# Optimization experiments

Hardware: AMD Instinct MI355X
Metric: run time of the kernel (lower is better)

Reference implementation:

```python
import jax, jax.numpy as jnp
import numpy as np

N_NODES = 50000
N_EDGES = 800000
NFEAT, NHID1, NHID2, NHID3, NCLASS = 128, 128, 128, 64, 32


def _glorot(key, fan_in, fan_out):
    lim = 1.0 / np.sqrt(fan_in)
    return jax.random.uniform(key, (fan_in, fan_out), jnp.float32, -lim, lim)


def setup_inputs() -> dict:
    key = jax.random.key(0)
    ks = jax.random.split(key, 12)
    x = jax.random.normal(ks[0], (N_NODES, NFEAT), jnp.float32)
    edge_src = jax.random.randint(ks[1], (N_EDGES,), 0, N_NODES, jnp.int32)
    edge_dst = jax.random.randint(ks[2], (N_EDGES,), 0, N_NODES, jnp.int32)
    edge_val = jax.random.uniform(ks[3], (N_EDGES,), jnp.float32)
    W1 = _glorot(ks[4], NFEAT, NHID1)
    W2 = _glorot(ks[5], NHID1, NHID2)
    W3 = _glorot(ks[6], NHID2, NHID3)
    W4 = _glorot(ks[7], NHID3, NCLASS)
    b1 = jnp.zeros((NHID1,), jnp.float32)
    b2 = jnp.zeros((NHID2,), jnp.float32)
    b3 = jnp.zeros((NHID3,), jnp.float32)
    b4 = jnp.zeros((NCLASS,), jnp.float32)
    return {"x": x, "edge_src": edge_src, "edge_dst": edge_dst, "edge_val": edge_val,
            "W1": W1, "b1": b1, "W2": W2, "b2": b2, "W3": W3, "b3": b3, "W4": W4, "b4": b4}


def _gc_layer(h, W, b, src, dst, val):
    # support = h @ W ; out = adj @ support + b  (adj in COO form)
    support = h @ W                                   # [N, d_out]
    msgs = support[src] * val[:, None]                # [E, d_out] irregular gather
    agg = jax.ops.segment_sum(msgs, dst, num_segments=N_NODES)  # scatter-add
    return agg + b


def reference(x, edge_src, edge_dst, edge_val, W1, b1, W2, b2, W3, b3, W4, b4):
    h = jax.nn.relu(_gc_layer(x, W1, b1, edge_src, edge_dst, edge_val))
    h = jax.nn.relu(_gc_layer(h, W2, b2, edge_src, edge_dst, edge_val))
    h = jax.nn.relu(_gc_layer(h, W3, b3, edge_src, edge_dst, edge_val))
    h = _gc_layer(h, W4, b4, edge_src, edge_dst, edge_val)
    return h
```

## Files before the change

### kernel.cpp

```cpp
#include <hip/hip_runtime.h>

constexpr int NNODES = 50000;
constexpr int NEDGES = 800000;
constexpr int CAP = 64;

typedef __attribute__((ext_vector_type(8))) short short8;
typedef __attribute__((ext_vector_type(8))) unsigned short ushort8;
typedef __attribute__((ext_vector_type(4))) float f32x4;

__device__ __forceinline__ unsigned short f2b(float f) {
    unsigned int u = __float_as_uint(f);
    u += 0x7FFFu + ((u >> 16) & 1u);
    return (unsigned short)(u >> 16);
}
__device__ __forceinline__ float b2f(unsigned short u) {
    return __uint_as_float(((unsigned int)u) << 16);
}

template <int N, int K>
__device__ __forceinline__ void pack_one(int idx, const float* __restrict__ W,
                                         unsigned short* __restrict__ Wp) {
    constexpr int KS = K / 32;
    int j = idx & 7;
    int lane = (idx >> 3) & 63;
    int t = idx >> 9;
    int nt = t / KS, ks = t % KS;
    int n = nt * 16 + (lane & 15);
    int k = ks * 32 + (lane >> 4) * 8 + j;
    Wp[idx] = f2b(W[(size_t)k * N + n]);
}

__global__ __launch_bounds__(256) void prep_kernel(int* __restrict__ cursor,
                                                   const float* __restrict__ W1,
                                                   const float* __restrict__ W2,
                                                   const float* __restrict__ W3,
                                                   const float* __restrict__ W4,
                                                   unsigned short* __restrict__ Wp1,
                                                   unsigned short* __restrict__ Wp2,
                                                   unsigned short* __restrict__ Wp3,
                                                   unsigned short* __restrict__ Wp4) {
    int idx = blockIdx.x * 256 + threadIdx.x;
    if (idx < NNODES) { cursor[idx] = 0; return; }
    int p = idx - NNODES;
    if (p < 16384) pack_one<128, 128>(p, W1, Wp1);
    else if (p < 32768) pack_one<128, 128>(p - 16384, W2, Wp2);
    else if (p < 40960) pack_one<64, 128>(p - 32768, W3, Wp3);
    else if (p < 43008) pack_one<32, 64>(p - 40960, W4, Wp4);
}

constexpr int NPART = 8;
constexpr int PSIZE = NNODES / NPART;
constexpr int FCH = 1024;
constexpr int QCAP = 320;

__global__ __launch_bounds__(256) void fill_kernel(const int* __restrict__ src,
                                                   const int* __restrict__ dst,
                                                   const float* __restrict__ val,
                                                   int* __restrict__ cursor,
                                                   int2* __restrict__ buckets) {
    __shared__ int q_e[QCAP];
    __shared__ int q_d[QCAP];
    __shared__ int qcount;
    if (threadIdx.x == 0) qcount = 0;
    __syncthreads();

    int part = blockIdx.x % NPART;
    int chunk = blockIdx.x / NPART;
    int lo = part * PSIZE, hi = lo + PSIZE;
    int e0 = chunk * FCH + threadIdx.x * 4;

    int4 d4 = make_int4(-1, -1, -1, -1);
    if (e0 + 3 < NEDGES) {
        d4 = *reinterpret_cast<const int4*>(dst + e0);
    } else if (e0 < NEDGES) {
        d4.x = dst[e0];
        if (e0 + 1 < NEDGES) d4.y = dst[e0 + 1];
        if (e0 + 2 < NEDGES) d4.z = dst[e0 + 2];
    }
    int dd[4] = {d4.x, d4.y, d4.z, d4.w};
#pragma unroll
    for (int i = 0; i < 4; ++i) {
        int d = dd[i];
        if (d >= lo && d < hi) {
            int pos = atomicAdd(&qcount, 1);
            if (pos < QCAP) {
                q_e[pos] = e0 + i;
                q_d[pos] = d;
            } else {
                int e = e0 + i;
                int p = atomicAdd(&cursor[d], 1);
                if (p < CAP)
                    buckets[(size_t)d * CAP + p] = make_int2(src[e], __float_as_int(val[e]));
            }
        }
    }
    __syncthreads();

    int n = qcount < QCAP ? qcount : QCAP;
    for (int i = threadIdx.x; i < n; i += 256) {
        int e = q_e[i];
        int d = q_d[i];
        int s = src[e];
        float v = val[e];
        int p = atomicAdd(&cursor[d], 1);
        if (p < CAP)
            buckets[(size_t)d * CAP + p] = make_int2(s, __float_as_int(v));
    }
}

template <int N, int K, bool AF32>
__global__ __launch_bounds__(256) void mfma_gemm_kernel(const void* __restrict__ Hv,
                                                        const unsigned short* __restrict__ Wp,
                                                        unsigned short* __restrict__ Sb) {
    constexpr int NT = N / 16, KS = K / 32;
    const int lane = threadIdx.x & 63;
    const int wave = threadIdx.x >> 6;
    const int waveRow = blockIdx.x * 64 + wave * 16;
    const int m = lane & 15, quad = lane >> 4;
    int arow = waveRow + m;
    if (arow >= NNODES) arow = NNODES - 1;

    f32x4 acc[NT];
#pragma unroll
    for (int nt = 0; nt < NT; ++nt) acc[nt] = (f32x4){0.f, 0.f, 0.f, 0.f};

#pragma unroll
    for (int ks = 0; ks < KS; ++ks) {
        short8 a;
        if (AF32) {
            const float* hp = (const float*)Hv + (size_t)arow * K + ks * 32 + quad * 8;
            float4 a0 = *reinterpret_cast<const float4*>(hp);
            float4 a1 = *reinterpret_cast<const float4*>(hp + 4);
            a[0] = (short)f2b(a0.x); a[1] = (short)f2b(a0.y);
            a[2] = (short)f2b(a0.z); a[3] = (short)f2b(a0.w);
            a[4] = (short)f2b(a1.x); a[5] = (short)f2b(a1.y);
            a[6] = (short)f2b(a1.z); a[7] = (short)f2b(a1.w);
        } else {
            a = *reinterpret_cast<const short8*>(
                (const unsigned short*)Hv + (size_t)arow * K + ks * 32 + quad * 8);
        }
#pragma unroll
        for (int nt = 0; nt < NT; ++nt) {
            short8 b = *reinterpret_cast<const short8*>(Wp + ((nt * KS + ks) * 64 + lane) * 8);
            acc[nt] = __builtin_amdgcn_mfma_f32_16x16x32_bf16(a, b, acc[nt], 0, 0, 0);
        }
    }

#pragma unroll
    for (int reg = 0; reg < 4; ++reg) {
        int grow = waveRow + quad * 4 + reg;
        if (grow < NNODES) {
#pragma unroll
            for (int nt = 0; nt < NT; ++nt)
                Sb[(size_t)grow * N + nt * 16 + m] = f2b(acc[nt][reg]);
        }
    }
}

template <int N, bool BOUT>
__global__ __launch_bounds__(256) void agg_kernel(const unsigned short* __restrict__ Sb,
                                                  const int2* __restrict__ buckets,
                                                  const int* __restrict__ counts,
                                                  const float* __restrict__ bias,
                                                  void* __restrict__ outp) {
    constexpr int NCH = N / 8;
    constexpr int NPB = 256 / NCH;
    int node = blockIdx.x * NPB + threadIdx.x / NCH;
    int cg = threadIdx.x % NCH;
    if (node >= NNODES) return;
    int cnt = counts[node];
    if (cnt > CAP) cnt = CAP;
    const int2* eb = buckets + (size_t)node * CAP;
    float acc[8];
#pragma unroll
    for (int t = 0; t < 8; ++t) acc[t] = bias[cg * 8 + t];

    int j = 0;
    for (; j + 4 <= cnt; j += 4) {
        int4 ea = *reinterpret_cast<const int4*>(eb + j);
        int4 ec = *reinterpret_cast<const int4*>(eb + j + 2);
        const ushort8 m0 = *reinterpret_cast<const ushort8*>(Sb + (size_t)ea.x * N + cg * 8);
        const ushort8 m1 = *reinterpret_cast<const ushort8*>(Sb + (size_t)ea.z * N + cg * 8);
        const ushort8 m2 = *reinterpret_cast<const ushort8*>(Sb + (size_t)ec.x * N + cg * 8);
        const ushort8 m3 = *reinterpret_cast<const ushort8*>(Sb + (size_t)ec.z * N + cg * 8);
        float v0 = __int_as_float(ea.y), v1 = __int_as_float(ea.w);
        float v2 = __int_as_float(ec.y), v3 = __int_as_float(ec.w);
#pragma unroll
        for (int t = 0; t < 8; ++t) {
            acc[t] = fmaf(b2f(m0[t]), v0, acc[t]);
            acc[t] = fmaf(b2f(m1[t]), v1, acc[t]);
            acc[t] = fmaf(b2f(m2[t]), v2, acc[t]);
            acc[t] = fmaf(b2f(m3[t]), v3, acc[t]);
        }
    }
    for (; j < cnt; ++j) {
        int2 e = eb[j];
        float v = __int_as_float(e.y);
        const ushort8 mr = *reinterpret_cast<const ushort8*>(Sb + (size_t)e.x * N + cg * 8);
#pragma unroll
        for (int t = 0; t < 8; ++t) acc[t] = fmaf(b2f(mr[t]), v, acc[t]);
    }

    if (BOUT) {
        ushort8 o;
#pragma unroll
        for (int t = 0; t < 8; ++t) o[t] = f2b(fmaxf(acc[t], 0.f));
        *reinterpret_cast<ushort8*>((unsigned short*)outp + (size_t)node * N + cg * 8) = o;
    } else {
        float* op = (float*)outp + (size_t)node * N + cg * 8;
        *reinterpret_cast<float4*>(op) = make_float4(acc[0], acc[1], acc[2], acc[3]);
        *reinterpret_cast<float4*>(op + 4) = make_float4(acc[4], acc[5], acc[6], acc[7]);
    }
}

extern "C" void kernel_launch(void* const* d_in, const int* in_sizes, int n_in,
                              void* d_out, int out_size, void* d_ws, size_t ws_size,
                              hipStream_t stream) {
    const float* x   = (const float*)d_in[0];
    const int*   src = (const int*)d_in[1];
    const int*   dst = (const int*)d_in[2];
    const float* val = (const float*)d_in[3];
    const float* W1  = (const float*)d_in[4];
    const float* b1  = (const float*)d_in[5];
    const float* W2  = (const float*)d_in[6];
    const float* b2  = (const float*)d_in[7];
    const float* W3  = (const float*)d_in[8];
    const float* b3  = (const float*)d_in[9];
    const float* W4  = (const float*)d_in[10];
    const float* b4  = (const float*)d_in[11];
    float* out = (float*)d_out;

    unsigned short* P = (unsigned short*)d_ws;
    unsigned short* Q = P + (size_t)NNODES * 128;
    int2* buckets = (int2*)(Q + (size_t)NNODES * 128);
    unsigned short* Wp1 = (unsigned short*)(buckets + (size_t)NNODES * CAP);
    unsigned short* Wp2 = Wp1 + 128 * 128;
    unsigned short* Wp3 = Wp2 + 128 * 128;
    unsigned short* Wp4 = Wp3 + 128 * 64;
    int* cursor = (int*)(Wp4 + 64 * 32);

    const dim3 blk(256);
    const int gemmGrid = (NNODES + 63) / 64;
    const int prepGrid = (NNODES + 43008 + 255) / 256;
    const int fillGrid = ((NEDGES + FCH - 1) / FCH) * NPART;

    prep_kernel<<<prepGrid, blk, 0, stream>>>(cursor, W1, W2, W3, W4, Wp1, Wp2, Wp3, Wp4);
    fill_kernel<<<fillGrid, blk, 0, stream>>>(src, dst, val, cursor, buckets);

    mfma_gemm_kernel<128, 128, true><<<gemmGrid, blk, 0, stream>>>(x, Wp1, Q);
    agg_kernel<128, true><<<(NNODES + 15) / 16, blk, 0, stream>>>(Q, buckets, cursor, b1, P);
    mfma_gemm_kernel<128, 128, false><<<gemmGrid, blk, 0, stream>>>(P, Wp2, Q);
    agg_kernel<128, true><<<(NNODES + 15) / 16, blk, 0, stream>>>(Q, buckets, cursor, b2, P);
    mfma_gemm_kernel<64, 128, false><<<gemmGrid, blk, 0, stream>>>(P, Wp3, Q);
    agg_kernel<64, true><<<(NNODES + 31) / 32, blk, 0, stream>>>(Q, buckets, cursor, b3, P);
    mfma_gemm_kernel<32, 64, false><<<gemmGrid, blk, 0, stream>>>(P, Wp4, Q);
    agg_kernel<32, false><<<(NNODES + 63) / 64, blk, 0, stream>>>(Q, buckets, cursor, b4, out);
}
```

Measured before the change: 254.0 us.

## Fuse aggregation of each layer with next layer's MFMA GEMM via LDS tile

Each aggregation (gather, scale, bias, ReLU) now writes its 64-node bf16 result into shared memory, and the same block immediately runs the next layer's MFMA GEMM from that tile. This removes the global round trip of the intermediate hidden activations and three kernel launches. In exchange, the gather now uses 4 threads per node with wider per-thread channel slices (more registers, fewer threads per node, less memory-level parallelism), and the GEMM waits on a block barrier.

Result: slower. 266.7 us (+5.0%).

```diff
diff --git a/kernel.cpp b/kernel.cpp
--- a/kernel.cpp
+++ b/kernel.cpp
@@ -108,10 +108,10 @@
     }
 }
 
-template <int N, int K, bool AF32>
-__global__ __launch_bounds__(256) void mfma_gemm_kernel(const void* __restrict__ Hv,
-                                                        const unsigned short* __restrict__ Wp,
-                                                        unsigned short* __restrict__ Sb) {
+template <int N, int K>
+__global__ __launch_bounds__(256) void mfma_gemm_f32_kernel(const float* __restrict__ H,
+                                                            const unsigned short* __restrict__ Wp,
+                                                            unsigned short* __restrict__ Sb) {
     constexpr int NT = N / 16, KS = K / 32;
     const int lane = threadIdx.x & 63;
     const int wave = threadIdx.x >> 6;
@@ -126,19 +126,14 @@
 
 #pragma unroll
     for (int ks = 0; ks < KS; ++ks) {
+        const float* hp = H + (size_t)arow * K + ks * 32 + quad * 8;
+        float4 a0 = *reinterpret_cast<const float4*>(hp);
+        float4 a1 = *reinterpret_cast<const float4*>(hp + 4);
         short8 a;
-        if (AF32) {
-            const float* hp = (const float*)Hv + (size_t)arow * K + ks * 32 + quad * 8;
-            float4 a0 = *reinterpret_cast<const float4*>(hp);
-            float4 a1 = *reinterpret_cast<const float4*>(hp + 4);
-            a[0] = (short)f2b(a0.x); a[1] = (short)f2b(a0.y);
-            a[2] = (short)f2b(a0.z); a[3] = (short)f2b(a0.w);
-            a[4] = (short)f2b(a1.x); a[5] = (short)f2b(a1.y);
-            a[6] = (short)f2b(a1.z); a[7] = (short)f2b(a1.w);
-        } else {
-            a = *reinterpret_cast<const short8*>(
-                (const unsigned short*)Hv + (size_t)arow * K + ks * 32 + quad * 8);
-        }
+        a[0] = (short)f2b(a0.x); a[1] = (short)f2b(a0.y);
+        a[2] = (short)f2b(a0.z); a[3] = (short)f2b(a0.w);
+        a[4] = (short)f2b(a1.x); a[5] = (short)f2b(a1.y);
+        a[6] = (short)f2b(a1.z); a[7] = (short)f2b(a1.w);
 #pragma unroll
         for (int nt = 0; nt < NT; ++nt) {
             short8 b = *reinterpret_cast<const short8*>(Wp + ((nt * KS + ks) * 64 + lane) * 8);
@@ -157,16 +152,116 @@
     }
 }
 
-template <int N, bool BOUT>
-__global__ __launch_bounds__(256) void agg_kernel(const unsigned short* __restrict__ Sb,
-                                                  const int2* __restrict__ buckets,
-                                                  const int* __restrict__ counts,
-                                                  const float* __restrict__ bias,
-                                                  void* __restrict__ outp) {
-    constexpr int NCH = N / 8;
-    constexpr int NPB = 256 / NCH;
-    int node = blockIdx.x * NPB + threadIdx.x / NCH;
-    int cg = threadIdx.x % NCH;
+template <int NIN, int NOUT>
+__global__ __launch_bounds__(256) void layer_kernel(const unsigned short* __restrict__ Sprev,
+                                                    const int2* __restrict__ buckets,
+                                                    const int* __restrict__ counts,
+                                                    const float* __restrict__ bias,
+                                                    const unsigned short* __restrict__ Wp,
+                                                    unsigned short* __restrict__ Snext) {
+    constexpr int KS = NIN / 32;
+    constexpr int NT = NOUT / 16;
+    constexpr int CPT = NIN / 4;
+    constexpr int NC8 = CPT / 8;
+    constexpr int LROW = NIN + 8;
+    __shared__ unsigned short htile[64 * LROW];
+
+    const int tid = threadIdx.x;
+    const int nodeBase = blockIdx.x * 64;
+
+    {
+        int nl = tid >> 2;
+        int q = tid & 3;
+        int node = nodeBase + nl;
+        float acc[CPT];
+        if (node < NNODES) {
+#pragma unroll
+            for (int t = 0; t < CPT; ++t) acc[t] = bias[q * CPT + t];
+            int cnt = counts[node];
+            if (cnt > CAP) cnt = CAP;
+            const int2* eb = buckets + (size_t)node * CAP;
+            int j = 0;
+            for (; j + 2 <= cnt; j += 2) {
+                int4 ee = *reinterpret_cast<const int4*>(eb + j);
+                const unsigned short* r0 = Sprev + (size_t)ee.x * NIN + q * CPT;
+                const unsigned short* r1 = Sprev + (size_t)ee.z * NIN + q * CPT;
+                ushort8 m0[NC8], m1[NC8];
+#pragma unroll
+                for (int c = 0; c < NC8; ++c) m0[c] = *reinterpret_cast<const ushort8*>(r0 + c * 8);
+#pragma unroll
+                for (int c = 0; c < NC8; ++c) m1[c] = *reinterpret_cast<const ushort8*>(r1 + c * 8);
+                float v0 = __int_as_float(ee.y), v1 = __int_as_float(ee.w);
+#pragma unroll
+                for (int c = 0; c < NC8; ++c)
+#pragma unroll
+                    for (int t = 0; t < 8; ++t) {
+                        acc[c * 8 + t] = fmaf(b2f(m0[c][t]), v0, acc[c * 8 + t]);
+                        acc[c * 8 + t] = fmaf(b2f(m1[c][t]), v1, acc[c * 8 + t]);
+                    }
+            }
+            if (j < cnt) {
+                int2 e = eb[j];
+                float v = __int_as_float(e.y);
+                const unsigned short* r0 = Sprev + (size_t)e.x * NIN + q * CPT;
+#pragma unroll
+                for (int c = 0; c < NC8; ++c) {
+                    ushort8 mr = *reinterpret_cast<const ushort8*>(r0 + c * 8);
+#pragma unroll
+                    for (int t = 0; t < 8; ++t)
+                        acc[c * 8 + t] = fmaf(b2f(mr[t]), v, acc[c * 8 + t]);
+                }
+            }
+        } else {
+#pragma unroll
+            for (int t = 0; t < CPT; ++t) acc[t] = 0.f;
+        }
+        unsigned short* lrow = &htile[nl * LROW + q * CPT];
+#pragma unroll
+        for (int c = 0; c < NC8; ++c) {
+            ushort8 o;
+#pragma unroll
+            for (int t = 0; t < 8; ++t) o[t] = f2b(fmaxf(acc[c * 8 + t], 0.f));
+            *reinterpret_cast<ushort8*>(lrow + c * 8) = o;
+        }
+    }
+    __syncthreads();
+
+    {
+        const int lane = tid & 63, wave = tid >> 6;
+        const int m = lane & 15, quad = lane >> 4;
+        const int lrow = wave * 16 + m;
+        f32x4 acc[NT];
+#pragma unroll
+        for (int nt = 0; nt < NT; ++nt) acc[nt] = (f32x4){0.f, 0.f, 0.f, 0.f};
+#pragma unroll
+        for (int ks = 0; ks < KS; ++ks) {
+            short8 a = *reinterpret_cast<const short8*>(&htile[lrow * LROW + ks * 32 + quad * 8]);
+#pragma unroll
+            for (int nt = 0; nt < NT; ++nt) {
+                short8 b = *reinterpret_cast<const short8*>(Wp + ((nt * KS + ks) * 64 + lane) * 8);
+                acc[nt] = __builtin_amdgcn_mfma_f32_16x16x32_bf16(a, b, acc[nt], 0, 0, 0);
+            }
+        }
+#pragma unroll
+        for (int reg = 0; reg < 4; ++reg) {
+            int grow = nodeBase + wave * 16 + quad * 4 + reg;
+            if (grow < NNODES) {
+#pragma unroll
+                for (int nt = 0; nt < NT; ++nt)
+                    Snext[(size_t)grow * NOUT + nt * 16 + m] = f2b(acc[nt][reg]);
+            }
+        }
+    }
+}
+
+__global__ __launch_bounds__(256) void agg_out_kernel(const unsigned short* __restrict__ Sb,
+                                                      const int2* __restrict__ buckets,
+                                                      const int* __restrict__ counts,
+                                                      const float* __restrict__ bias,
+                                                      float* __restrict__ outp) {
+    constexpr int N = 32;
+    int node = blockIdx.x * 64 + threadIdx.x / 4;
+    int cg = threadIdx.x % 4;
     if (node >= NNODES) return;
     int cnt = counts[node];
     if (cnt > CAP) cnt = CAP;
@@ -201,16 +296,9 @@
         for (int t = 0; t < 8; ++t) acc[t] = fmaf(b2f(mr[t]), v, acc[t]);
     }
 
-    if (BOUT) {
-        ushort8 o;
-#pragma unroll
-        for (int t = 0; t < 8; ++t) o[t] = f2b(fmaxf(acc[t], 0.f));
-        *reinterpret_cast<ushort8*>((unsigned short*)outp + (size_t)node * N + cg * 8) = o;
-    } else {
-        float* op = (float*)outp + (size_t)node * N + cg * 8;
-        *reinterpret_cast<float4*>(op) = make_float4(acc[0], acc[1], acc[2], acc[3]);
-        *reinterpret_cast<float4*>(op + 4) = make_float4(acc[4], acc[5], acc[6], acc[7]);
-    }
+    float* op = outp + (size_t)node * N + cg * 8;
+    *reinterpret_cast<float4*>(op) = make_float4(acc[0], acc[1], acc[2], acc[3]);
+    *reinterpret_cast<float4*>(op + 4) = make_float4(acc[4], acc[5], acc[6], acc[7]);
 }
 
 extern "C" void kernel_launch(void* const* d_in, const int* in_sizes, int n_in,
@@ -240,19 +328,16 @@
     int* cursor = (int*)(Wp4 + 64 * 32);
 
     const dim3 blk(256);
-    const int gemmGrid = (NNODES + 63) / 64;
+    const int grid64 = (NNODES + 63) / 64;
     const int prepGrid = (NNODES + 43008 + 255) / 256;
     const int fillGrid = ((NEDGES + FCH - 1) / FCH) * NPART;
 
     prep_kernel<<<prepGrid, blk, 0, stream>>>(cursor, W1, W2, W3, W4, Wp1, Wp2, Wp3, Wp4);
     fill_kernel<<<fillGrid, blk, 0, stream>>>(src, dst, val, cursor, buckets);
 
-    mfma_gemm_kernel<128, 128, true><<<gemmGrid, blk, 0, stream>>>(x, Wp1, Q);
-    agg_kernel<128, true><<<(NNODES + 15) / 16, blk, 0, stream>>>(Q, buckets, cursor, b1, P);
-    mfma_gemm_kernel<128, 128, false><<<gemmGrid, blk, 0, stream>>>(P, Wp2, Q);
-    agg_kernel<128, true><<<(NNODES + 15) / 16, blk, 0, stream>>>(Q, buckets, cursor, b2, P);
-    mfma_gemm_kernel<64, 128, false><<<gemmGrid, blk, 0, stream>>>(P, Wp3, Q);
-    agg_kernel<64, true><<<(NNODES + 31) / 32, blk, 0, stream>>>(Q, buckets, cursor, b3, P);
-    mfma_gemm_kernel<32, 64, false><<<gemmGrid, blk, 0, stream>>>(P, Wp4, Q);
-    agg_kernel<32, false><<<(NNODES + 63) / 64, blk, 0, stream>>>(Q, buckets, cursor, b4, out);
-}
+    mfma_gemm_f32_kernel<128, 128><<<grid64, blk, 0, stream>>>(x, Wp1, Q);
+    layer_kernel<128, 128><<<grid64, blk, 0, stream>>>(Q, buckets, cursor, b1, Wp2, P);
+    layer_kernel<128, 64><<<grid64, blk, 0, stream>>>(P, buckets, cursor, b2, Wp3, Q);
+    layer_kernel<64, 32><<<grid64, blk, 0, stream>>>(Q, buckets, cursor, b3, Wp4, P);
+    agg_out_kernel<<<grid64, blk, 0, stream>>>(P, buckets, cursor, b4, out);
+}
```

## Fuse all GCN stages into one persistent cooperative kernel with grid syncs

Applied to the files above, without the earlier changes.

Replaces the ten separate launches with one persistent cooperative kernel. Blocks loop over work items for each stage, with grid-wide barriers between stages. The bucket fill and the first-layer GEMM now share one stage, since they are independent. The aim is to remove per-launch overhead and tail gaps between small kernels. The cost is grid.sync barriers, a fixed grid of at most 1024 blocks, and occupancy capped by launch bounds. The old multi-kernel path is kept as a fallback if the cooperative launch fails.

Measured after the change: 794.7 us. 3.13x slower.

```diff
diff --git a/kernel.cpp b/kernel.cpp
--- a/kernel.cpp
+++ b/kernel.cpp
@@ -1,8 +1,20 @@
 #include <hip/hip_runtime.h>
+#include <hip/hip_cooperative_groups.h>
+
+namespace cg = cooperative_groups;
 
 constexpr int NNODES = 50000;
 constexpr int NEDGES = 800000;
 constexpr int CAP = 64;
+
+constexpr int NPART = 8;
+constexpr int PSIZE = NNODES / NPART;
+constexpr int FCH = 1024;
+constexpr int QCAP = 320;
+
+constexpr int FILL_ITEMS = ((NEDGES + FCH - 1) / FCH) * NPART;
+constexpr int TILE_ITEMS = (NNODES + 63) / 64;
+constexpr int PREP_TOT = NNODES + 43008;
 
 typedef __attribute__((ext_vector_type(8))) short short8;
 typedef __attribute__((ext_vector_type(8))) unsigned short ushort8;
@@ -30,16 +42,11 @@
     Wp[idx] = f2b(W[(size_t)k * N + n]);
 }
 
-__global__ __launch_bounds__(256) void prep_kernel(int* __restrict__ cursor,
-                                                   const float* __restrict__ W1,
-                                                   const float* __restrict__ W2,
-                                                   const float* __restrict__ W3,
-                                                   const float* __restrict__ W4,
-                                                   unsigned short* __restrict__ Wp1,
-                                                   unsigned short* __restrict__ Wp2,
-                                                   unsigned short* __restrict__ Wp3,
-                                                   unsigned short* __restrict__ Wp4) {
-    int idx = blockIdx.x * 256 + threadIdx.x;
+__device__ __forceinline__ void prep_elem(int idx, int* __restrict__ cursor,
+                                          const float* W1, const float* W2,
+                                          const float* W3, const float* W4,
+                                          unsigned short* Wp1, unsigned short* Wp2,
+                                          unsigned short* Wp3, unsigned short* Wp4) {
     if (idx < NNODES) { cursor[idx] = 0; return; }
     int p = idx - NNODES;
     if (p < 16384) pack_one<128, 128>(p, W1, Wp1);
@@ -48,24 +55,17 @@
     else if (p < 43008) pack_one<32, 64>(p - 40960, W4, Wp4);
 }
 
-constexpr int NPART = 8;
-constexpr int PSIZE = NNODES / NPART;
-constexpr int FCH = 1024;
-constexpr int QCAP = 320;
-
-__global__ __launch_bounds__(256) void fill_kernel(const int* __restrict__ src,
-                                                   const int* __restrict__ dst,
-                                                   const float* __restrict__ val,
-                                                   int* __restrict__ cursor,
-                                                   int2* __restrict__ buckets) {
-    __shared__ int q_e[QCAP];
-    __shared__ int q_d[QCAP];
-    __shared__ int qcount;
-    if (threadIdx.x == 0) qcount = 0;
+__device__ __forceinline__ void fill_item(int w, const int* __restrict__ src,
+                                          const int* __restrict__ dst,
+                                          const float* __restrict__ val,
+                                          int* __restrict__ cursor,
+                                          int2* __restrict__ buckets,
+                                          int* q_e, int* q_d, int* qcount) {
+    if (threadIdx.x == 0) *qcount = 0;
     __syncthreads();
 
-    int part = blockIdx.x % NPART;
-    int chunk = blockIdx.x / NPART;
+    int part = w % NPART;
+    int chunk = w / NPART;
     int lo = part * PSIZE, hi = lo + PSIZE;
     int e0 = chunk * FCH + threadIdx.x * 4;
 
@@ -82,7 +82,7 @@
     for (int i = 0; i < 4; ++i) {
         int d = dd[i];
         if (d >= lo && d < hi) {
-            int pos = atomicAdd(&qcount, 1);
+            int pos = atomicAdd(qcount, 1);
             if (pos < QCAP) {
                 q_e[pos] = e0 + i;
                 q_d[pos] = d;
@@ -96,7 +96,7 @@
     }
     __syncthreads();
 
-    int n = qcount < QCAP ? qcount : QCAP;
+    int n = *qcount < QCAP ? *qcount : QCAP;
     for (int i = threadIdx.x; i < n; i += 256) {
         int e = q_e[i];
         int d = q_d[i];
@@ -109,13 +109,13 @@
 }
 
 template <int N, int K, bool AF32>
-__global__ __launch_bounds__(256) void mfma_gemm_kernel(const void* __restrict__ Hv,
-                                                        const unsigned short* __restrict__ Wp,
-                                                        unsigned short* __restrict__ Sb) {
+__device__ __forceinline__ void gemm_item(int t, const void* __restrict__ Hv,
+                                          const unsigned short* __restrict__ Wp,
+                                          unsigned short* __restrict__ Sb) {
     constexpr int NT = N / 16, KS = K / 32;
     const int lane = threadIdx.x & 63;
     const int wave = threadIdx.x >> 6;
-    const int waveRow = blockIdx.x * 64 + wave * 16;
+    const int waveRow = t * 64 + wave * 16;
     const int m = lane & 15, quad = lane >> 4;
     int arow = waveRow + m;
     if (arow >= NNODES) arow = NNODES - 1;
@@ -158,31 +158,31 @@
 }
 
 template <int N, bool BOUT>
-__global__ __launch_bounds__(256) void agg_kernel(const unsigned short* __restrict__ Sb,
-                                                  const int2* __restrict__ buckets,
-                                                  const int* __restrict__ counts,
-                                                  const float* __restrict__ bias,
-                                                  void* __restrict__ outp) {
+__device__ __forceinline__ void agg_item(int w, const unsigned short* __restrict__ Sb,
+                                         const int2* __restrict__ buckets,
+                                         const int* __restrict__ counts,
+                                         const float* __restrict__ bias,
+                                         void* __restrict__ outp) {
     constexpr int NCH = N / 8;
     constexpr int NPB = 256 / NCH;
-    int node = blockIdx.x * NPB + threadIdx.x / NCH;
-    int cg = threadIdx.x % NCH;
+    int node = w * NPB + threadIdx.x / NCH;
+    int cgi = threadIdx.x % NCH;
     if (node >= NNODES) return;
     int cnt = counts[node];
     if (cnt > CAP) cnt = CAP;
     const int2* eb = buckets + (size_t)node * CAP;
     float acc[8];
 #pragma unroll
-    for (int t = 0; t < 8; ++t) acc[t] = bias[cg * 8 + t];
+    for (int t = 0; t < 8; ++t) acc[t] = bias[cgi * 8 + t];
 
     int j = 0;
     for (; j + 4 <= cnt; j += 4) {
         int4 ea = *reinterpret_cast<const int4*>(eb + j);
         int4 ec = *reinterpret_cast<const int4*>(eb + j + 2);
-        const ushort8 m0 = *reinterpret_cast<const ushort8*>(Sb + (size_t)ea.x * N + cg * 8);
-        const ushort8 m1 = *reinterpret_cast<const ushort8*>(Sb + (size_t)ea.z * N + cg * 8);
-        const ushort8 m2 = *reinterpret_cast<const ushort8*>(Sb + (size_t)ec.x * N + cg * 8);
-        const ushort8 m3 = *reinterpret_cast<const ushort8*>(Sb + (size_t)ec.z * N + cg * 8);
+        const ushort8 m0 = *reinterpret_cast<const ushort8*>(Sb + (size_t)ea.x * N + cgi * 8);
+        const ushort8 m1 = *reinterpret_cast<const ushort8*>(Sb + (size_t)ea.z * N + cgi * 8);
+        const ushort8 m2 = *reinterpret_cast<const ushort8*>(Sb + (size_t)ec.x * N + cgi * 8);
+        const ushort8 m3 = *reinterpret_cast<const ushort8*>(Sb + (size_t)ec.z * N + cgi * 8);
         float v0 = __int_as_float(ea.y), v1 = __int_as_float(ea.w);
         float v2 = __int_as_float(ec.y), v3 = __int_as_float(ec.w);
 #pragma unroll
@@ -196,7 +196,7 @@
     for (; j < cnt; ++j) {
         int2 e = eb[j];
         float v = __int_as_float(e.y);
-        const ushort8 mr = *reinterpret_cast<const ushort8*>(Sb + (size_t)e.x * N + cg * 8);
+        const ushort8 mr = *reinterpret_cast<const ushort8*>(Sb + (size_t)e.x * N + cgi * 8);
 #pragma unroll
         for (int t = 0; t < 8; ++t) acc[t] = fmaf(b2f(mr[t]), v, acc[t]);
     }
@@ -205,12 +205,99 @@
         ushort8 o;
 #pragma unroll
         for (int t = 0; t < 8; ++t) o[t] = f2b(fmaxf(acc[t], 0.f));
-        *reinterpret_cast<ushort8*>((unsigned short*)outp + (size_t)node * N + cg * 8) = o;
+        *reinterpret_cast<ushort8*>((unsigned short*)outp + (size_t)node * N + cgi * 8) = o;
     } else {
-        float* op = (float*)outp + (size_t)node * N + cg * 8;
+        float* op = (float*)outp + (size_t)node * N + cgi * 8;
         *reinterpret_cast<float4*>(op) = make_float4(acc[0], acc[1], acc[2], acc[3]);
         *reinterpret_cast<float4*>(op + 4) = make_float4(acc[4], acc[5], acc[6], acc[7]);
     }
+}
+
+__global__ __launch_bounds__(256, 4) void mono_kernel(
+        const float* __restrict__ x, const int* __restrict__ src,
+        const int* __restrict__ dst, const float* __restrict__ val,
+        const float* __restrict__ W1, const float* __restrict__ b1,
+        const float* __restrict__ W2, const float* __restrict__ b2,
+        const float* __restrict__ W3, const float* __restrict__ b3,
+        const float* __restrict__ W4, const float* __restrict__ b4,
+        float* __restrict__ out,
+        unsigned short* __restrict__ P, unsigned short* __restrict__ Q,
+        int2* __restrict__ buckets,
+        unsigned short* __restrict__ Wp1, unsigned short* __restrict__ Wp2,
+        unsigned short* __restrict__ Wp3, unsigned short* __restrict__ Wp4,
+        int* __restrict__ cursor) {
+    cg::grid_group grid = cg::this_grid();
+    const int nb = gridDim.x;
+    __shared__ int q_e[QCAP];
+    __shared__ int q_d[QCAP];
+    __shared__ int qcount;
+
+    for (int base = blockIdx.x * 256; base < PREP_TOT; base += nb * 256) {
+        int idx = base + threadIdx.x;
+        if (idx < PREP_TOT)
+            prep_elem(idx, cursor, W1, W2, W3, W4, Wp1, Wp2, Wp3, Wp4);
+    }
+    grid.sync();
+
+    for (int w = blockIdx.x; w < FILL_ITEMS + TILE_ITEMS; w += nb) {
+        if (w < FILL_ITEMS) fill_item(w, src, dst, val, cursor, buckets, q_e, q_d, &qcount);
+        else gemm_item<128, 128, true>(w - FILL_ITEMS, x, Wp1, Q);
+    }
+    grid.sync();
+
+    for (int w = blockIdx.x; w < (NNODES + 15) / 16; w += nb)
+        agg_item<128, true>(w, Q, buckets, cursor, b1, P);
+    grid.sync();
+
+    for (int w = blockIdx.x; w < TILE_ITEMS; w += nb)
+        gemm_item<128, 128, false>(w, P, Wp2, Q);
+    grid.sync();
+
+    for (int w = blockIdx.x; w < (NNODES + 15) / 16; w += nb)
+        agg_item<128, true>(w, Q, buckets, cursor, b2, P);
+    grid.sync();
+
+    for (int w = blockIdx.x; w < TILE_ITEMS; w += nb)
+        gemm_item<64, 128, false>(w, P, Wp3, Q);
+    grid.sync();
+
+    for (int w = blockIdx.x; w < (NNODES + 31) / 32; w += nb)
+        agg_item<64, true>(w, Q, buckets, cursor, b3, P);
+    grid.sync();
+
+    for (int w = blockIdx.x; w < TILE_ITEMS; w += nb)
+        gemm_item<32, 64, false>(w, P, Wp4, Q);
+    grid.sync();
+
+    for (int w = blockIdx.x; w < (NNODES + 63) / 64; w += nb)
+        agg_item<32, false>(w, Q, buckets, cursor, b4, out);
+}
+
+__global__ __launch_bounds__(256) void prep_kernel(int* cursor,
+        const float* W1, const float* W2, const float* W3, const float* W4,
+        unsigned short* Wp1, unsigned short* Wp2, unsigned short* Wp3, unsigned short* Wp4) {
+    int idx = blockIdx.x * 256 + threadIdx.x;
+    if (idx < PREP_TOT) prep_elem(idx, cursor, W1, W2, W3, W4, Wp1, Wp2, Wp3, Wp4);
+}
+
+__global__ __launch_bounds__(256) void fill_kernel(const int* src, const int* dst,
+        const float* val, int* cursor, int2* buckets) {
+    __shared__ int q_e[QCAP];
+    __shared__ int q_d[QCAP];
+    __shared__ int qcount;
+    fill_item(blockIdx.x, src, dst, val, cursor, buckets, q_e, q_d, &qcount);
+}
+
+template <int N, int K, bool AF32>
+__global__ __launch_bounds__(256) void gemm_kernel(const void* Hv,
+        const unsigned short* Wp, unsigned short* Sb) {
+    gemm_item<N, K, AF32>(blockIdx.x, Hv, Wp, Sb);
+}
+
+template <int N, bool BOUT>
+__global__ __launch_bounds__(256) void agg_kernel(const unsigned short* Sb,
+        const int2* buckets, const int* counts, const float* bias, void* outp) {
+    agg_item<N, BOUT>(blockIdx.x, Sb, buckets, counts, bias, outp);
 }
 
 extern "C" void kernel_launch(void* const* d_in, const int* in_sizes, int n_in,
@@ -239,20 +326,33 @@
     unsigned short* Wp4 = Wp3 + 128 * 64;
     int* cursor = (int*)(Wp4 + 64 * 32);
 
+    int blocksPerCU = 0;
+    hipError_t occErr = hipOccupancyMaxActiveBlocksPerMultiprocessor(
+        &blocksPerCU, (const void*)mono_kernel, 256, 0);
+    if (occErr == hipSuccess && blocksPerCU > 0) {
+        int grid = blocksPerCU * 256;
+        if (grid > 1024) grid = 1024;
+        void* args[] = {(void*)&x, (void*)&src, (void*)&dst, (void*)&val,
+                        (void*)&W1, (void*)&b1, (void*)&W2, (void*)&b2,
+                        (void*)&W3, (void*)&b3, (void*)&W4, (void*)&b4,
+                        (void*)&out, (void*)&P, (void*)&Q, (void*)&buckets,
+                        (void*)&Wp1, (void*)&Wp2, (void*)&Wp3, (void*)&Wp4,
+                        (void*)&cursor};
+        hipError_t err = hipLaunchCooperativeKernel((const void*)mono_kernel,
+                                                    dim3(grid), dim3(256), args, 0, stream);
+        if (err == hipSuccess) return;
+    }
+
     const dim3 blk(256);
-    const int gemmGrid = (NNODES + 63) / 64;
-    const int prepGrid = (NNODES + 43008 + 255) / 256;
-    const int fillGrid = ((NEDGES + FCH - 1) / FCH) * NPART;
-
-    prep_kernel<<<prepGrid, blk, 0, stream>>>(cursor, W1, W2, W3, W4, Wp1, Wp2, Wp3, Wp4);
-    fill_kernel<<<fillGrid, blk, 0, stream>>>(src, dst, val, cursor, buckets);
-
-    mfma_gemm_kernel<128, 128, true><<<gemmGrid, blk, 0, stream>>>(x, Wp1, Q);
+    prep_kernel<<<(PREP_TOT + 255) / 256, blk, 0, stream>>>(cursor, W1, W2, W3, W4,
+                                                            Wp1, Wp2, Wp3, Wp4);
+    fill_kernel<<<FILL_ITEMS, blk, 0, stream>>>(src, dst, val, cursor, buckets);
+    gemm_kernel<128, 128, true><<<TILE_ITEMS, blk, 0, stream>>>(x, Wp1, Q);
     agg_kernel<128, true><<<(NNODES + 15) / 16, blk, 0, stream>>>(Q, buckets, cursor, b1, P);
-    mfma_gemm_kernel<128, 128, false><<<gemmGrid, blk, 0, stream>>>(P, Wp2, Q);
+    gemm_kernel<128, 128, false><<<TILE_ITEMS, blk, 0, stream>>>(P, Wp2, Q);
     agg_kernel<128, true><<<(NNODES + 15) / 16, blk, 0, stream>>>(Q, buckets, cursor, b2, P);
-    mfma_gemm_kernel<64, 128, false><<<gemmGrid, blk, 0, stream>>>(P, Wp3, Q);
+    gemm_kernel<64, 128, false><<<TILE_ITEMS, blk, 0, stream>>>(P, Wp3, Q);
     agg_kernel<64, true><<<(NNODES + 31) / 32, blk, 0, stream>>>(Q, buckets, cursor, b3, P);
-    mfma_gemm_kernel<32, 64, false><<<gemmGrid, blk, 0, stream>>>(P, Wp4, Q);
+    gemm_kernel<32, 64, false><<<TILE_ITEMS, blk, 0, stream>>>(P, Wp4, Q);
     agg_kernel<32, false><<<(NNODES + 63) / 64, blk, 0, stream>>>(Q, buckets, cursor, b4, out);
 }
```

## Fuse aggregation with next-layer GEMM and merge edge fill with first GEMM

Applied to the files above, without the earlier changes.

Each aggregation kernel now writes its ReLU'd bf16 result into a shared-memory tile and immediately runs the next layer's MFMA GEMM on it. This removes the round trip of hidden activations through global memory and cuts the launch count. The edge-bucket fill and the first-layer GEMM are merged into one launch, with extra blocks doing the GEMM tiles so both run concurrently. The cost is small 16- or 32-row GEMM tiles per block, with the weights re-read from global by every block and more LDS use per block.

Measured after the change: 227.2 us. 1.12x faster.

```diff
diff --git a/kernel.cpp b/kernel.cpp
--- a/kernel.cpp
+++ b/kernel.cpp
@@ -3,6 +3,15 @@
 constexpr int NNODES = 50000;
 constexpr int NEDGES = 800000;
 constexpr int CAP = 64;
+
+constexpr int NPART = 8;
+constexpr int PSIZE = NNODES / NPART;
+constexpr int FCH = 1024;
+constexpr int QCAP = 320;
+
+constexpr int FILL_ITEMS = ((NEDGES + FCH - 1) / FCH) * NPART;
+constexpr int TILE_ITEMS = (NNODES + 63) / 64;
+constexpr int PREP_TOT = NNODES + 43008;
 
 typedef __attribute__((ext_vector_type(8))) short short8;
 typedef __attribute__((ext_vector_type(8))) unsigned short ushort8;
@@ -31,91 +40,27 @@
 }
 
 __global__ __launch_bounds__(256) void prep_kernel(int* __restrict__ cursor,
-                                                   const float* __restrict__ W1,
-                                                   const float* __restrict__ W2,
-                                                   const float* __restrict__ W3,
-                                                   const float* __restrict__ W4,
-                                                   unsigned short* __restrict__ Wp1,
-                                                   unsigned short* __restrict__ Wp2,
-                                                   unsigned short* __restrict__ Wp3,
-                                                   unsigned short* __restrict__ Wp4) {
+        const float* __restrict__ W1, const float* __restrict__ W2,
+        const float* __restrict__ W3, const float* __restrict__ W4,
+        unsigned short* __restrict__ Wp1, unsigned short* __restrict__ Wp2,
+        unsigned short* __restrict__ Wp3, unsigned short* __restrict__ Wp4) {
     int idx = blockIdx.x * 256 + threadIdx.x;
     if (idx < NNODES) { cursor[idx] = 0; return; }
     int p = idx - NNODES;
     if (p < 16384) pack_one<128, 128>(p, W1, Wp1);
     else if (p < 32768) pack_one<128, 128>(p - 16384, W2, Wp2);
     else if (p < 40960) pack_one<64, 128>(p - 32768, W3, Wp3);
-    else if (p < 43008) pack_one<32, 64>(p - 40960, W4, Wp4);
-}
-
-constexpr int NPART = 8;
-constexpr int PSIZE = NNODES / NPART;
-constexpr int FCH = 1024;
-constexpr int QCAP = 320;
-
-__global__ __launch_bounds__(256) void fill_kernel(const int* __restrict__ src,
-                                                   const int* __restrict__ dst,
-                                                   const float* __restrict__ val,
-                                                   int* __restrict__ cursor,
-                                                   int2* __restrict__ buckets) {
-    __shared__ int q_e[QCAP];
-    __shared__ int q_d[QCAP];
-    __shared__ int qcount;
-    if (threadIdx.x == 0) qcount = 0;
-    __syncthreads();
-
-    int part = blockIdx.x % NPART;
-    int chunk = blockIdx.x / NPART;
-    int lo = part * PSIZE, hi = lo + PSIZE;
-    int e0 = chunk * FCH + threadIdx.x * 4;
-
-    int4 d4 = make_int4(-1, -1, -1, -1);
-    if (e0 + 3 < NEDGES) {
-        d4 = *reinterpret_cast<const int4*>(dst + e0);
-    } else if (e0 < NEDGES) {
-        d4.x = dst[e0];
-        if (e0 + 1 < NEDGES) d4.y = dst[e0 + 1];
-        if (e0 + 2 < NEDGES) d4.z = dst[e0 + 2];
-    }
-    int dd[4] = {d4.x, d4.y, d4.z, d4.w};
-#pragma unroll
-    for (int i = 0; i < 4; ++i) {
-        int d = dd[i];
-        if (d >= lo && d < hi) {
-            int pos = atomicAdd(&qcount, 1);
-            if (pos < QCAP) {
-                q_e[pos] = e0 + i;
-                q_d[pos] = d;
-            } else {
-                int e = e0 + i;
-                int p = atomicAdd(&cursor[d], 1);
-                if (p < CAP)
-                    buckets[(size_t)d * CAP + p] = make_int2(src[e], __float_as_int(val[e]));
-            }
-        }
-    }
-    __syncthreads();
-
-    int n = qcount < QCAP ? qcount : QCAP;
-    for (int i = threadIdx.x; i < n; i += 256) {
-        int e = q_e[i];
-        int d = q_d[i];
-        int s = src[e];
-        float v = val[e];
-        int p = atomicAdd(&cursor[d], 1);
-        if (p < CAP)
-            buckets[(size_t)d * CAP + p] = make_int2(s, __float_as_int(v));
-    }
+    else if (p < 43008 && p >= 40960) pack_one<32, 64>(p - 40960, W4, Wp4);
 }
 
 template <int N, int K, bool AF32>
-__global__ __launch_bounds__(256) void mfma_gemm_kernel(const void* __restrict__ Hv,
-                                                        const unsigned short* __restrict__ Wp,
-                                                        unsigned short* __restrict__ Sb) {
+__device__ __forceinline__ void gemm_item(int t, const void* __restrict__ Hv,
+                                          const unsigned short* __restrict__ Wp,
+                                          unsigned short* __restrict__ Sb) {
     constexpr int NT = N / 16, KS = K / 32;
     const int lane = threadIdx.x & 63;
     const int wave = threadIdx.x >> 6;
-    const int waveRow = blockIdx.x * 64 + wave * 16;
+    const int waveRow = t * 64 + wave * 16;
     const int m = lane & 15, quad = lane >> 4;
     int arow = waveRow + m;
     if (arow >= NNODES) arow = NNODES - 1;
@@ -157,16 +102,160 @@
     }
 }
 
-template <int N, bool BOUT>
-__global__ __launch_bounds__(256) void agg_kernel(const unsigned short* __restrict__ Sb,
-                                                  const int2* __restrict__ buckets,
-                                                  const int* __restrict__ counts,
-                                                  const float* __restrict__ bias,
-                                                  void* __restrict__ outp) {
-    constexpr int NCH = N / 8;
-    constexpr int NPB = 256 / NCH;
-    int node = blockIdx.x * NPB + threadIdx.x / NCH;
-    int cg = threadIdx.x % NCH;
+__global__ __launch_bounds__(256) void fill_gemm1_kernel(
+        const int* __restrict__ src, const int* __restrict__ dst,
+        const float* __restrict__ val, int* __restrict__ cursor,
+        int2* __restrict__ buckets,
+        const float* __restrict__ x, const unsigned short* __restrict__ Wp1,
+        unsigned short* __restrict__ Q) {
+    __shared__ int q_e[QCAP];
+    __shared__ int q_d[QCAP];
+    __shared__ int qcount;
+
+    if (blockIdx.x >= FILL_ITEMS) {
+        gemm_item<128, 128, true>(blockIdx.x - FILL_ITEMS, x, Wp1, Q);
+        return;
+    }
+
+    if (threadIdx.x == 0) qcount = 0;
+    __syncthreads();
+
+    int part = blockIdx.x % NPART;
+    int chunk = blockIdx.x / NPART;
+    int lo = part * PSIZE, hi = lo + PSIZE;
+    int e0 = chunk * FCH + threadIdx.x * 4;
+
+    int4 d4 = make_int4(-1, -1, -1, -1);
+    if (e0 + 3 < NEDGES) {
+        d4 = *reinterpret_cast<const int4*>(dst + e0);
+    } else if (e0 < NEDGES) {
+        d4.x = dst[e0];
+        if (e0 + 1 < NEDGES) d4.y = dst[e0 + 1];
+        if (e0 + 2 < NEDGES) d4.z = dst[e0 + 2];
+    }
+    int dd[4] = {d4.x, d4.y, d4.z, d4.w};
+#pragma unroll
+    for (int i = 0; i < 4; ++i) {
+        int d = dd[i];
+        if (d >= lo && d < hi) {
+            int pos = atomicAdd(&qcount, 1);
+            if (pos < QCAP) {
+                q_e[pos] = e0 + i;
+                q_d[pos] = d;
+            } else {
+                int e = e0 + i;
+                int p = atomicAdd(&cursor[d], 1);
+                if (p < CAP)
+                    buckets[(size_t)d * CAP + p] = make_int2(src[e], __float_as_int(val[e]));
+            }
+        }
+    }
+    __syncthreads();
+
+    int n = qcount < QCAP ? qcount : QCAP;
+    for (int i = threadIdx.x; i < n; i += 256) {
+        int e = q_e[i];
+        int d = q_d[i];
+        int s = src[e];
+        float v = val[e];
+        int p = atomicAdd(&cursor[d], 1);
+        if (p < CAP)
+            buckets[(size_t)d * CAP + p] = make_int2(s, __float_as_int(v));
+    }
+}
+
+template <int NIN, int NOUT>
+__global__ __launch_bounds__(256) void agg_gemm_kernel(
+        const unsigned short* __restrict__ Sprev, const int2* __restrict__ buckets,
+        const int* __restrict__ counts, const float* __restrict__ bias,
+        const unsigned short* __restrict__ Wp, unsigned short* __restrict__ Snext) {
+    constexpr int NCH = NIN / 8;
+    constexpr int R = 256 / NCH;
+    constexpr int LROW = NIN + 8;
+    constexpr int KS = NIN / 32;
+    constexpr int NT = NOUT / 16;
+    constexpr int RT = R / 16;
+    constexpr int TILES = RT * NT;
+    __shared__ unsigned short htile[R * LROW];
+
+    const int nodeBase = blockIdx.x * R;
+
+    {
+        int nl = threadIdx.x / NCH;
+        int cg = threadIdx.x % NCH;
+        int node = nodeBase + nl;
+        float acc[8];
+        if (node < NNODES) {
+#pragma unroll
+            for (int t = 0; t < 8; ++t) acc[t] = bias[cg * 8 + t];
+            int cnt = counts[node];
+            if (cnt > CAP) cnt = CAP;
+            const int2* eb = buckets + (size_t)node * CAP;
+            int j = 0;
+            for (; j + 4 <= cnt; j += 4) {
+                int4 ea = *reinterpret_cast<const int4*>(eb + j);
+                int4 ec = *reinterpret_cast<const int4*>(eb + j + 2);
+                const ushort8 m0 = *reinterpret_cast<const ushort8*>(Sprev + (size_t)ea.x * NIN + cg * 8);
+                const ushort8 m1 = *reinterpret_cast<const ushort8*>(Sprev + (size_t)ea.z * NIN + cg * 8);
+                const ushort8 m2 = *reinterpret_cast<const ushort8*>(Sprev + (size_t)ec.x * NIN + cg * 8);
+                const ushort8 m3 = *reinterpret_cast<const ushort8*>(Sprev + (size_t)ec.z * NIN + cg * 8);
+                float v0 = __int_as_float(ea.y), v1 = __int_as_float(ea.w);
+                float v2 = __int_as_float(ec.y), v3 = __int_as_float(ec.w);
+#pragma unroll
+                for (int t = 0; t < 8; ++t) {
+                    acc[t] = fmaf(b2f(m0[t]), v0, acc[t]);
+                    acc[t] = fmaf(b2f(m1[t]), v1, acc[t]);
+                    acc[t] = fmaf(b2f(m2[t]), v2, acc[t]);
+                    acc[t] = fmaf(b2f(m3[t]), v3, acc[t]);
+                }
+            }
+            for (; j < cnt; ++j) {
+                int2 e = eb[j];
+                float v = __int_as_float(e.y);
+                const ushort8 mr = *reinterpret_cast<const ushort8*>(Sprev + (size_t)e.x * NIN + cg * 8);
+#pragma unroll
+                for (int t = 0; t < 8; ++t) acc[t] = fmaf(b2f(mr[t]), v, acc[t]);
+            }
+        } else {
+#pragma unroll
+            for (int t = 0; t < 8; ++t) acc[t] = 0.f;
+        }
+        ushort8 o;
+#pragma unroll
+        for (int t = 0; t < 8; ++t) o[t] = f2b(fmaxf(acc[t], 0.f));
+        *reinterpret_cast<ushort8*>(&htile[nl * LROW + cg * 8]) = o;
+    }
+    __syncthreads();
+
+    {
+        const int lane = threadIdx.x & 63, wave = threadIdx.x >> 6;
+        const int m = lane & 15, quad = lane >> 4;
+        for (int t = wave; t < TILES; t += 4) {
+            int rt = t / NT, nt = t % NT;
+            f32x4 acc = (f32x4){0.f, 0.f, 0.f, 0.f};
+#pragma unroll
+            for (int ks = 0; ks < KS; ++ks) {
+                short8 a = *reinterpret_cast<const short8*>(
+                    &htile[(rt * 16 + m) * LROW + ks * 32 + quad * 8]);
+                short8 b = *reinterpret_cast<const short8*>(Wp + ((nt * KS + ks) * 64 + lane) * 8);
+                acc = __builtin_amdgcn_mfma_f32_16x16x32_bf16(a, b, acc, 0, 0, 0);
+            }
+#pragma unroll
+            for (int reg = 0; reg < 4; ++reg) {
+                int grow = nodeBase + rt * 16 + quad * 4 + reg;
+                if (grow < NNODES)
+                    Snext[(size_t)grow * NOUT + nt * 16 + m] = f2b(acc[reg]);
+            }
+        }
+    }
+}
+
+__global__ __launch_bounds__(256) void agg_out_kernel(const unsigned short* __restrict__ Sb,
+        const int2* __restrict__ buckets, const int* __restrict__ counts,
+        const float* __restrict__ bias, float* __restrict__ outp) {
+    constexpr int N = 32;
+    int node = blockIdx.x * 64 + threadIdx.x / 4;
+    int cg = threadIdx.x % 4;
     if (node >= NNODES) return;
     int cnt = counts[node];
     if (cnt > CAP) cnt = CAP;
@@ -201,16 +290,9 @@
         for (int t = 0; t < 8; ++t) acc[t] = fmaf(b2f(mr[t]), v, acc[t]);
     }
 
-    if (BOUT) {
-        ushort8 o;
-#pragma unroll
-        for (int t = 0; t < 8; ++t) o[t] = f2b(fmaxf(acc[t], 0.f));
-        *reinterpret_cast<ushort8*>((unsigned short*)outp + (size_t)node * N + cg * 8) = o;
-    } else {
-        float* op = (float*)outp + (size_t)node * N + cg * 8;
-        *reinterpret_cast<float4*>(op) = make_float4(acc[0], acc[1], acc[2], acc[3]);
-        *reinterpret_cast<float4*>(op + 4) = make_float4(acc[4], acc[5], acc[6], acc[7]);
-    }
+    float* op = outp + (size_t)node * N + cg * 8;
+    *reinterpret_cast<float4*>(op) = make_float4(acc[0], acc[1], acc[2], acc[3]);
+    *reinterpret_cast<float4*>(op + 4) = make_float4(acc[4], acc[5], acc[6], acc[7]);
 }
 
 extern "C" void kernel_launch(void* const* d_in, const int* in_sizes, int n_in,
@@ -240,19 +322,16 @@
     int* cursor = (int*)(Wp4 + 64 * 32);
 
     const dim3 blk(256);
-    const int gemmGrid = (NNODES + 63) / 64;
-    const int prepGrid = (NNODES + 43008 + 255) / 256;
-    const int fillGrid = ((NEDGES + FCH - 1) / FCH) * NPART;
-
-    prep_kernel<<<prepGrid, blk, 0, stream>>>(cursor, W1, W2, W3, W4, Wp1, Wp2, Wp3, Wp4);
-    fill_kernel<<<fillGrid, blk, 0, stream>>>(src, dst, val, cursor, buckets);
-
-    mfma_gemm_kernel<128, 128, true><<<gemmGrid, blk, 0, stream>>>(x, Wp1, Q);
-    agg_kernel<128, true><<<(NNODES + 15) / 16, blk, 0, stream>>>(Q, buckets, cursor, b1, P);
-    mfma_gemm_kernel<128, 128, false><<<gemmGrid, blk, 0, stream>>>(P, Wp2, Q);
-    agg_kernel<128, true><<<(NNODES + 15) / 16, blk, 0, stream>>>(Q, buckets, cursor, b2, P);
-    mfma_gemm_kernel<64, 128, false><<<gemmGrid, blk, 0, stream>>>(P, Wp3, Q);
-    agg_kernel<64, true><<<(NNODES + 31) / 32, blk, 0, stream>>>(Q, buckets, cursor, b3, P);
-    mfma_gemm_kernel<32, 64, false><<<gemmGrid, blk, 0, stream>>>(P, Wp4, Q);
-    agg_kernel<32, false><<<(NNODES + 63) / 64, blk, 0, stream>>>(Q, buckets, cursor, b4, out);
-}
+
+    prep_kernel<<<(PREP_TOT + 255) / 256, blk, 0, stream>>>(cursor, W1, W2, W3, W4,
+                                                            Wp1, Wp2, Wp3, Wp4);
+    fill_gemm1_kernel<<<FILL_ITEMS + TILE_ITEMS, blk, 0, stream>>>(
+        src, dst, val, cursor, buckets, x, Wp1, Q);
+    agg_gemm_kernel<128, 128><<<(NNODES + 15) / 16, blk, 0, stream>>>(
+        Q, buckets, cursor, b1, Wp2, P);
+    agg_gemm_kernel<128, 64><<<(NNODES + 15) / 16, blk, 0, stream>>>(
+        P, buckets, cursor, b2, Wp3, Q);
+    agg_gemm_kernel<64, 32><<<(NNODES + 31) / 32, blk, 0, stream>>>(
+        Q, buckets, cursor, b3, Wp4, P);
+    agg_out_kernel<<<(NNODES + 63) / 64, blk, 0, stream>>>(P, buckets, cursor, b4, out);
+}
```
